# Kernel tuning notes

Hardware: AMD Instinct MI355X
Metric: run time of the kernel (lower is better)

## Reference

```python
import jax, jax.numpy as jnp
import numpy as np

EPS = 1e-5

def _bn2d(x, g, b, m, v):
    s = (1, -1, 1, 1)
    return (x - m.reshape(s)) * (g.reshape(s) * jax.lax.rsqrt(v.reshape(s) + EPS)) + b.reshape(s)

def _bn1d(x, g, b, m, v):
    return (x - m) * (g * jax.lax.rsqrt(v + EPS)) + b

def _conv3x3(x, w, b):
    y = jax.lax.conv_general_dilated(x, w, (1, 1), ((1, 1), (1, 1)),
                                     dimension_numbers=('NCHW', 'OIHW', 'NCHW'))
    return y + b.reshape(1, -1, 1, 1)

def setup_inputs() -> dict:
    key = jax.random.key(0)
    ks = iter(jax.random.split(key, 64))
    B = 512
    d = {}
    d['anchor'] = jax.random.normal(next(ks), (B, 1, 16, 8), jnp.float32)
    d['positive'] = jax.random.normal(next(ks), (B, 1, 16, 8), jnp.float32)
    d['negative'] = jax.random.normal(next(ks), (B, 1, 16, 8), jnp.float32)

    def bn_params(c):
        g = jax.random.normal(next(ks), (c,), jnp.float32) * 0.1 + 1.0
        b = jax.random.normal(next(ks), (c,), jnp.float32) * 0.1
        m = jax.random.normal(next(ks), (c,), jnp.float32) * 0.1
        v = jax.random.uniform(next(ks), (c,), jnp.float32, 0.5, 1.5)
        return g, b, m, v

    d['bn0_g'], d['bn0_b'], d['bn0_m'], d['bn0_v'] = bn_params(1)
    d['conv1_w'] = jax.random.normal(next(ks), (64, 1, 3, 3), jnp.float32) * 0.1
    d['conv1_b'] = jax.random.normal(next(ks), (64,), jnp.float32) * 0.1
    d['bn1_g'], d['bn1_b'], d['bn1_m'], d['bn1_v'] = bn_params(64)
    d['conv2_w'] = jax.random.normal(next(ks), (64, 64, 3, 3), jnp.float32) * 0.04
    d['conv2_b'] = jax.random.normal(next(ks), (64,), jnp.float32) * 0.1
    d['bn2_g'], d['bn2_b'], d['bn2_m'], d['bn2_v'] = bn_params(64)
    # locally-connected: kernel_size=1 -> per-position unshared channel mix (o,c,h,w)
    d['lc1_w'] = jax.random.normal(next(ks), (64, 64, 16, 8), jnp.float32) * 0.125
    d['bn3_g'], d['bn3_b'], d['bn3_m'], d['bn3_v'] = bn_params(64)
    d['lc2_w'] = jax.random.normal(next(ks), (64, 64, 16, 8), jnp.float32) * 0.125
    d['bn4_g'], d['bn4_b'], d['bn4_m'], d['bn4_v'] = bn_params(64)
    d['fc1_w'] = jax.random.normal(next(ks), (512, 8192), jnp.float32) * 0.01
    d['fc1_b'] = jax.random.normal(next(ks), (512,), jnp.float32) * 0.1
    d['bnf1_g'], d['bnf1_b'], d['bnf1_m'], d['bnf1_v'] = bn_params(512)
    d['fc2_w'] = jax.random.normal(next(ks), (512, 512), jnp.float32) * 0.04
    d['fc2_b'] = jax.random.normal(next(ks), (512,), jnp.float32) * 0.1
    d['bnf2_g'], d['bnf2_b'], d['bnf2_m'], d['bnf2_v'] = bn_params(512)
    d['fc3_w'] = jax.random.normal(next(ks), (128, 512), jnp.float32) * 0.04
    d['fc3_b'] = jax.random.normal(next(ks), (128,), jnp.float32) * 0.1
    d['bnf3_g'], d['bnf3_b'], d['bnf3_m'], d['bnf3_v'] = bn_params(128)
    d['out_w'] = jax.random.normal(next(ks), (128, 128), jnp.float32) * 0.09
    d['out_b'] = jax.random.normal(next(ks), (128,), jnp.float32) * 0.1
    return d

def _embedding(x, p):
    x = _bn2d(x, p['bn0_g'], p['bn0_b'], p['bn0_m'], p['bn0_v'])
    x = _conv3x3(x, p['conv1_w'], p['conv1_b'])
    x = jax.nn.relu(_bn2d(x, p['bn1_g'], p['bn1_b'], p['bn1_m'], p['bn1_v']))
    x = _conv3x3(x, p['conv2_w'], p['conv2_b'])
    x = jax.nn.relu(_bn2d(x, p['bn2_g'], p['bn2_b'], p['bn2_m'], p['bn2_v']))
    # locally connected (kernel 1): per-position channel mix, no huge unfold intermediate
    x = jnp.einsum('bchw,ochw->bohw', x, p['lc1_w'])
    x = jax.nn.relu(_bn2d(x, p['bn3_g'], p['bn3_b'], p['bn3_m'], p['bn3_v']))
    x = jnp.einsum('bchw,ochw->bohw', x, p['lc2_w'])
    x = jax.nn.relu(_bn2d(x, p['bn4_g'], p['bn4_b'], p['bn4_m'], p['bn4_v']))
    # dropout is identity in eval mode
    x = x.reshape(x.shape[0], -1)  # (B, 8192)
    x = x @ p['fc1_w'].T + p['fc1_b']
    x = jax.nn.relu(_bn1d(x, p['bnf1_g'], p['bnf1_b'], p['bnf1_m'], p['bnf1_v']))
    x = x @ p['fc2_w'].T + p['fc2_b']
    x = jax.nn.relu(_bn1d(x, p['bnf2_g'], p['bnf2_b'], p['bnf2_m'], p['bnf2_v']))
    x = x @ p['fc3_w'].T + p['fc3_b']
    x = jax.nn.relu(_bn1d(x, p['bnf3_g'], p['bnf3_b'], p['bnf3_m'], p['bnf3_v']))
    return x @ p['out_w'].T + p['out_b']

def reference(anchor, positive, negative,
              bn0_g, bn0_b, bn0_m, bn0_v,
              conv1_w, conv1_b, bn1_g, bn1_b, bn1_m, bn1_v,
              conv2_w, conv2_b, bn2_g, bn2_b, bn2_m, bn2_v,
              lc1_w, bn3_g, bn3_b, bn3_m, bn3_v,
              lc2_w, bn4_g, bn4_b, bn4_m, bn4_v,
              fc1_w, fc1_b, bnf1_g, bnf1_b, bnf1_m, bnf1_v,
              fc2_w, fc2_b, bnf2_g, bnf2_b, bnf2_m, bnf2_v,
              fc3_w, fc3_b, bnf3_g, bnf3_b, bnf3_m, bnf3_v,
              out_w, out_b):
    p = dict(bn0_g=bn0_g, bn0_b=bn0_b, bn0_m=bn0_m, bn0_v=bn0_v,
             conv1_w=conv1_w, conv1_b=conv1_b, bn1_g=bn1_g, bn1_b=bn1_b, bn1_m=bn1_m, bn1_v=bn1_v,
             conv2_w=conv2_w, conv2_b=conv2_b, bn2_g=bn2_g, bn2_b=bn2_b, bn2_m=bn2_m, bn2_v=bn2_v,
             lc1_w=lc1_w, bn3_g=bn3_g, bn3_b=bn3_b, bn3_m=bn3_m, bn3_v=bn3_v,
             lc2_w=lc2_w, bn4_g=bn4_g, bn4_b=bn4_b, bn4_m=bn4_m, bn4_v=bn4_v,
             fc1_w=fc1_w, fc1_b=fc1_b, bnf1_g=bnf1_g, bnf1_b=bnf1_b, bnf1_m=bnf1_m, bnf1_v=bnf1_v,
             fc2_w=fc2_w, fc2_b=fc2_b, bnf2_g=bnf2_g, bnf2_b=bnf2_b, bnf2_m=bnf2_m, bnf2_v=bnf2_v,
             fc3_w=fc3_w, fc3_b=fc3_b, bnf3_g=bnf3_g, bnf3_b=bnf3_b, bnf3_m=bnf3_m, bnf3_v=bnf3_v,
             out_w=out_w, out_b=out_b)
    return (_embedding(anchor, p), _embedding(positive, p), _embedding(negative, p))
```

## Files before the change

### kernel.cpp

```cpp
#include <hip/hip_runtime.h>
#include <math.h>

#define EPS 1e-5f
#define FD 8192

typedef __attribute__((ext_vector_type(8))) __bf16 bf16x8;
typedef __attribute__((ext_vector_type(4))) float f32x4;

static __device__ __forceinline__ f32x4 mfma16(bf16x8 a, bf16x8 b, f32x4 c) {
    return __builtin_amdgcn_mfma_f32_16x16x32_bf16(a, b, c, 0, 0, 0);
}

__global__ void k_prep_w1frag(const float* __restrict__ w1, __bf16* __restrict__ out) {
    const int t = threadIdx.x;
    const int lane = t & 63, w = t >> 6;
    const int q = lane >> 4, li = lane & 15;
    const int o = w * 16 + li;
    bf16x8 v;
#pragma unroll
    for (int j = 0; j < 8; ++j) {
        int k = q * 8 + j;
        v[j] = (k < 9) ? (__bf16)w1[o * 9 + k] : (__bf16)0.0f;
    }
    *(bf16x8*)(out + t * 8) = v;
}

__global__ void k_prep_w2frag(const float* __restrict__ w2, __bf16* __restrict__ out) {
    const int id = blockIdx.x * 256 + threadIdx.x;
    const int lane = id & 63;
    const int w = (id >> 6) & 3;
    const int chunk = (id >> 8) & 1;
    const int tap = id >> 9;
    const int q = lane >> 4, li = lane & 15;
    const int o = w * 16 + li;
    const int c0 = chunk * 32 + q * 8;
    bf16x8 v;
#pragma unroll
    for (int j = 0; j < 8; ++j)
        v[j] = (__bf16)w2[(o * 64 + c0 + j) * 9 + tap];
    *(bf16x8*)(out + (size_t)id * 8) = v;
}

__global__ __launch_bounds__(256) void k_prep_lcT(const float* __restrict__ lc1,
                                                  const float* __restrict__ lc2,
                                                  __bf16* __restrict__ o1,
                                                  __bf16* __restrict__ o2) {
    const int bx = blockIdx.x;
    const int layer = bx >> 6, o = bx & 63;
    const int wo = o >> 4, lo = o & 15;
    const int t = threadIdx.x;
    const float* src = (layer ? lc2 : lc1) + (size_t)o * 8192;
    __bf16* dst = layer ? o2 : o1;
    __shared__ float wbuf[64][130];
#pragma unroll
    for (int pass = 0; pass < 8; ++pass) {
        int i = pass * 1024 + t * 4;
        float4 v = *(const float4*)(src + i);
        int c = i >> 7, p = i & 127;
        wbuf[c][p + 0] = v.x; wbuf[c][p + 1] = v.y;
        wbuf[c][p + 2] = v.z; wbuf[c][p + 3] = v.w;
    }
    __syncthreads();
#pragma unroll
    for (int pass = 0; pass < 4; ++pass) {
        int slot = pass * 256 + t;
        int p = slot >> 3, chunk = (slot >> 2) & 1, q = slot & 3;
        bf16x8 v;
#pragma unroll
        for (int j = 0; j < 8; ++j)
            v[j] = (__bf16)wbuf[chunk * 32 + q * 8 + j][p];
        *(bf16x8*)(dst + ((size_t)((p * 2 + chunk) * 4 + wo) * 64 + q * 16 + lo) * 8) = v;
    }
}

__global__ __launch_bounds__(256) void k_prep_fc1T(const float* __restrict__ fw,
                                                   __bf16* __restrict__ out) {
    const int n = blockIdx.x;
    const int t = threadIdx.x;
    const float* src = fw + (size_t)n * 8192;
    __bf16* dst = out + (size_t)n * 8192;
    __shared__ float wbuf[64][130];
#pragma unroll
    for (int pass = 0; pass < 8; ++pass) {
        int i = pass * 1024 + t * 4;
        float4 v = *(const float4*)(src + i);
        int c = i >> 7, p = i & 127;
        wbuf[c][p + 0] = v.x; wbuf[c][p + 1] = v.y;
        wbuf[c][p + 2] = v.z; wbuf[c][p + 3] = v.w;
    }
    __syncthreads();
#pragma unroll
    for (int pass = 0; pass < 16; ++pass) {
        int kA = (pass * 256 + t) * 2;
        int c = kA & 63, p = kA >> 6;
        __bf16 tmp[2];
        tmp[0] = (__bf16)wbuf[c][p];
        tmp[1] = (__bf16)wbuf[c + 1][p];
        *(unsigned int*)(dst + kA) = *(unsigned int*)tmp;
    }
}

__global__ void k_cvt3(const float* __restrict__ w2, const float* __restrict__ w3,
                       const float* __restrict__ wo, __bf16* __restrict__ dst) {
    int i = blockIdx.x * 256 + threadIdx.x;
    if (i >= 344064) return;
    float v;
    if (i < 262144) v = w2[i];
    else if (i < 327680) v = w3[i - 262144];
    else v = wo[i - 327680];
    dst[i] = (__bf16)v;
}

__global__ __launch_bounds__(256) void k_conv_mfma(
    const float* __restrict__ inA, const float* __restrict__ inP, const float* __restrict__ inN,
    const float* __restrict__ bn0g, const float* __restrict__ bn0b,
    const float* __restrict__ bn0m, const float* __restrict__ bn0v,
    const __bf16* __restrict__ w1frag, const float* __restrict__ b1,
    const float* __restrict__ bn1g, const float* __restrict__ bn1b,
    const float* __restrict__ bn1m, const float* __restrict__ bn1v,
    const __bf16* __restrict__ w2frag, const float* __restrict__ b2,
    const float* __restrict__ bn2g, const float* __restrict__ bn2b,
    const float* __restrict__ bn2m, const float* __restrict__ bn2v,
    __bf16* __restrict__ act) {
    const int b = blockIdx.x, t = threadIdx.x;
    const int lane = t & 63, w = t >> 6;
    const int q = lane >> 4, li = lane & 15;
    const int n0 = w * 16;
    const float* src = (b < 512 ? inA : (b < 1024 ? inP : inN)) + (size_t)(b & 511) * 128;

    __shared__ __align__(16) float xpad[180];
    __shared__ __align__(16) __bf16 A1[128 * 40];
    __shared__ __align__(16) __bf16 Xp[18 * 12 * 72];
    __shared__ float s1[64], sh1[64], s2[64], sh2[64];

    bf16x8 w1f = *(const bf16x8*)(w1frag + (size_t)(w * 64 + lane) * 8);
    bf16x8 w2f[18];
#pragma unroll
    for (int tap = 0; tap < 9; ++tap)
#pragma unroll
        for (int ch = 0; ch < 2; ++ch)
            w2f[tap * 2 + ch] = *(const bf16x8*)(w2frag +
                ((size_t)((tap * 2 + ch) * 4 + w) * 64 + lane) * 8);

    {
        int* xz = (int*)Xp;
        for (int i = t; i < 7776; i += 256) xz[i] = 0;
        if (t < 180) xpad[t] = 0.f;
        if (t < 64) {
            float sa = bn1g[t] * rsqrtf(bn1v[t] + EPS);
            s1[t] = sa;
            sh1[t] = (b1[t] - bn1m[t]) * sa + bn1b[t];
            float sb = bn2g[t] * rsqrtf(bn2v[t] + EPS);
            s2[t] = sb;
            sh2[t] = (b2[t] - bn2m[t]) * sb + bn2b[t];
        }
    }
    __syncthreads();
    if (t < 128) {
        float s0 = bn0g[0] * rsqrtf(bn0v[0] + EPS);
        float v = (src[t] - bn0m[0]) * s0 + bn0b[0];
        xpad[((t >> 3) + 1) * 10 + (t & 7) + 1] = v;
    }
    __syncthreads();
    {
        int p = t >> 1, jh = (t & 1) * 16;
        int r = p >> 3, cl = p & 7;
#pragma unroll
        for (int jj = 0; jj < 16; ++jj) {
            int j = jh + jj;
            float v = 0.f;
            if (j < 9) v = xpad[(r + j / 3) * 10 + cl + (j % 3)];
            A1[p * 40 + j] = (__bf16)v;
        }
    }
    __syncthreads();
    {
        const float sco = s1[n0 + li], sho = sh1[n0 + li];
        const int o = n0 + li;
#pragma unroll
        for (int m = 0; m < 8; ++m) {
            bf16x8 a = *(const bf16x8*)&A1[(m * 16 + li) * 40 + q * 8];
            f32x4 z = {0.f, 0.f, 0.f, 0.f};
            f32x4 d = mfma16(a, w1f, z);
#pragma unroll
            for (int r = 0; r < 4; ++r) {
                int p = m * 16 + q * 4 + r;
                float v = fmaxf(d[r] * sco + sho, 0.f);
                Xp[(((p >> 3) + 1) * 12 + (p & 7) + 1) * 72 + o] = (__bf16)v;
            }
        }
    }
    __syncthreads();
    {
        const float sco = s2[n0 + li], sho = sh2[n0 + li];
        const int o = n0 + li;
        const int cl = li & 7;
#pragma unroll
        for (int mp = 0; mp < 4; ++mp) {
            const int m0t = mp * 2;
            const int r0 = m0t * 2 + (li >> 3);
            const int base0 = (r0 * 12 + cl) * 72 + q * 8;
            const int base1 = base0 + 1728;
            f32x4 acc0 = {0.f, 0.f, 0.f, 0.f};
            f32x4 acc1 = {0.f, 0.f, 0.f, 0.f};
#pragma unroll
            for (int tap = 0; tap < 9; ++tap) {
                const int tofs = ((tap / 3) * 12 + (tap % 3)) * 72;
#pragma unroll
                for (int ch = 0; ch < 2; ++ch) {
                    bf16x8 a0 = *(const bf16x8*)&Xp[base0 + tofs + ch * 32];
                    bf16x8 a1 = *(const bf16x8*)&Xp[base1 + tofs + ch * 32];
                    acc0 = mfma16(a0, w2f[tap * 2 + ch], acc0);
                    acc1 = mfma16(a1, w2f[tap * 2 + ch], acc1);
                }
            }
            __bf16* ob = act + (size_t)b * FD + o;
#pragma unroll
            for (int r = 0; r < 4; ++r) {
                int p0 = m0t * 16 + q * 4 + r;
                ob[p0 * 64] = (__bf16)fmaxf(acc0[r] * sco + sho, 0.f);
                ob[(p0 + 16) * 64] = (__bf16)fmaxf(acc1[r] * sco + sho, 0.f);
            }
        }
    }
}

__global__ __launch_bounds__(256) void k_lc_mfma(
    const __bf16* __restrict__ lc1frag, const __bf16* __restrict__ lc2frag,
    const float* __restrict__ bn3g, const float* __restrict__ bn3b,
    const float* __restrict__ bn3m, const float* __restrict__ bn3v,
    const float* __restrict__ bn4g, const float* __restrict__ bn4b,
    const float* __restrict__ bn4m, const float* __restrict__ bn4v,
    __bf16* __restrict__ act) {
    const int p = blockIdx.x;
    const int b0 = blockIdx.y * 64;
    const int t = threadIdx.x;
    const int lane = t & 63, w = t >> 6;
    const int q = lane >> 4, li = lane & 15;
    const int n0 = w * 16;

    __shared__ __align__(16) __bf16 xs[64 * 72];
    __shared__ __align__(16) __bf16 ys[64 * 72];
    __shared__ float s3[64], sh3[64], s4[64], sh4[64];

    if (t < 64) {
        float sa = bn3g[t] * rsqrtf(bn3v[t] + EPS);
        s3[t] = sa; sh3[t] = bn3b[t] - bn3m[t] * sa;
        float sb = bn4g[t] * rsqrtf(bn4v[t] + EPS);
        s4[t] = sb; sh4[t] = bn4b[t] - bn4m[t] * sb;
    }
    {
        int s = t >> 2, cg = t & 3;
        const __bf16* rp = act + (size_t)(b0 + s) * FD + p * 64 + cg * 16;
        *(bf16x8*)&xs[s * 72 + cg * 16] = *(const bf16x8*)rp;
        *(bf16x8*)&xs[s * 72 + cg * 16 + 8] = *(const bf16x8*)(rp + 8);
    }
    bf16x8 w1a = *(const bf16x8*)(lc1frag + ((size_t)((p * 2 + 0) * 4 + w) * 64 + lane) * 8);
    bf16x8 w1b = *(const bf16x8*)(lc1frag + ((size_t)((p * 2 + 1) * 4 + w) * 64 + lane) * 8);
    bf16x8 w2a = *(const bf16x8*)(lc2frag + ((size_t)((p * 2 + 0) * 4 + w) * 64 + lane) * 8);
    bf16x8 w2b = *(const bf16x8*)(lc2frag + ((size_t)((p * 2 + 1) * 4 + w) * 64 + lane) * 8);
    __syncthreads();
    {
        const float sco = s3[n0 + li], sho = sh3[n0 + li];
#pragma unroll
        for (int m = 0; m < 4; ++m) {
            bf16x8 a0 = *(const bf16x8*)&xs[(m * 16 + li) * 72 + q * 8];
            bf16x8 a1 = *(const bf16x8*)&xs[(m * 16 + li) * 72 + 32 + q * 8];
            f32x4 acc = {0.f, 0.f, 0.f, 0.f};
            acc = mfma16(a0, w1a, acc);
            acc = mfma16(a1, w1b, acc);
#pragma unroll
            for (int r = 0; r < 4; ++r) {
                int bl = m * 16 + q * 4 + r;
                ys[bl * 72 + n0 + li] = (__bf16)fmaxf(acc[r] * sco + sho, 0.f);
            }
        }
    }
    __syncthreads();
    {
        const float sco = s4[n0 + li], sho = sh4[n0 + li];
#pragma unroll
        for (int m = 0; m < 4; ++m) {
            bf16x8 a0 = *(const bf16x8*)&ys[(m * 16 + li) * 72 + q * 8];
            bf16x8 a1 = *(const bf16x8*)&ys[(m * 16 + li) * 72 + 32 + q * 8];
            f32x4 acc = {0.f, 0.f, 0.f, 0.f};
            acc = mfma16(a0, w2a, acc);
            acc = mfma16(a1, w2b, acc);
#pragma unroll
            for (int r = 0; r < 4; ++r) {
                int bl = m * 16 + q * 4 + r;
                act[(size_t)(b0 + bl) * FD + p * 64 + n0 + li] =
                    (__bf16)fmaxf(acc[r] * sco + sho, 0.f);
            }
        }
    }
}

__global__ __launch_bounds__(256) void k_fc1_mfma(
    const __bf16* __restrict__ A, const __bf16* __restrict__ Wb,
    float* __restrict__ part) {
    const int t = threadIdx.x;
    const int lane = t & 63, w = t >> 6;
    const int q = lane >> 4, li = lane & 15;
    const int m0 = blockIdx.x * 64, n0 = blockIdx.y * 128;
    const int k0 = blockIdx.z * 1024;
    const int wm = (w & 1) * 32, wn = (w >> 1) * 64;

    __shared__ __align__(16) __bf16 As[64 * 40];
    __shared__ __align__(16) __bf16 Bs[128 * 40];

    f32x4 acc[2][4];
#pragma unroll
    for (int i = 0; i < 2; ++i)
#pragma unroll
        for (int j = 0; j < 4; ++j) acc[i][j] = (f32x4){0.f, 0.f, 0.f, 0.f};

    const int rowA = (t & 127) >> 1, rowB = t >> 1, half = t & 1;
    const __bf16* Ag = A + (size_t)(m0 + rowA) * 8192 + k0 + half * 16;
    const __bf16* Bg = Wb + (size_t)(n0 + rowB) * 8192 + k0 + half * 16;

    for (int step = 0; step < 32; ++step) {
        bf16x8 b0 = *(const bf16x8*)Bg;
        bf16x8 b1 = *(const bf16x8*)(Bg + 8);
        if (t < 128) {
            bf16x8 a0 = *(const bf16x8*)Ag;
            bf16x8 a1 = *(const bf16x8*)(Ag + 8);
            *(bf16x8*)&As[rowA * 40 + half * 16] = a0;
            *(bf16x8*)&As[rowA * 40 + half * 16 + 8] = a1;
        }
        *(bf16x8*)&Bs[rowB * 40 + half * 16] = b0;
        *(bf16x8*)&Bs[rowB * 40 + half * 16 + 8] = b1;
        __syncthreads();
        bf16x8 af[2], bfr[4];
#pragma unroll
        for (int i = 0; i < 2; ++i)
            af[i] = *(const bf16x8*)&As[(wm + i * 16 + li) * 40 + q * 8];
#pragma unroll
        for (int j = 0; j < 4; ++j)
            bfr[j] = *(const bf16x8*)&Bs[(wn + j * 16 + li) * 40 + q * 8];
#pragma unroll
        for (int i = 0; i < 2; ++i)
#pragma unroll
            for (int j = 0; j < 4; ++j)
                acc[i][j] = mfma16(af[i], bfr[j], acc[i][j]);
        __syncthreads();
        Ag += 32;
        Bg += 32;
    }
    float* pp = part + (size_t)blockIdx.z * 786432;
#pragma unroll
    for (int i = 0; i < 2; ++i) {
#pragma unroll
        for (int r = 0; r < 4; ++r) {
            int m = m0 + wm + i * 16 + q * 4 + r;
#pragma unroll
            for (int j = 0; j < 4; ++j) {
                int n = n0 + wn + j * 16 + li;
                pp[(size_t)m * 512 + n] = acc[i][j][r];
            }
        }
    }
}

__global__ void k_fc1_reduce(const float* __restrict__ part, const float* __restrict__ bias,
                             const float* __restrict__ g, const float* __restrict__ bb,
                             const float* __restrict__ mm, const float* __restrict__ vv,
                             __bf16* __restrict__ out) {
    int gi = blockIdx.x * 256 + threadIdx.x;
    size_t off = (size_t)gi * 4;
    float4 s = make_float4(0.f, 0.f, 0.f, 0.f);
#pragma unroll
    for (int z = 0; z < 8; ++z) {
        float4 v = *(const float4*)(part + (size_t)z * 786432 + off);
        s.x += v.x; s.y += v.y; s.z += v.z; s.w += v.w;
    }
    int n = (gi & 127) * 4;
    float r[4] = {s.x, s.y, s.z, s.w};
    __bf16 o4[4];
#pragma unroll
    for (int j = 0; j < 4; ++j) {
        float sc = g[n + j] * rsqrtf(vv[n + j] + EPS);
        float x = (r[j] + bias[n + j] - mm[n + j]) * sc + bb[n + j];
        o4[j] = (__bf16)fmaxf(x, 0.f);
    }
    *(uint2*)(out + off) = *(uint2*)o4;
}

template <int FINAL>
__global__ __launch_bounds__(256) void k_fc_mfma(
    const __bf16* __restrict__ A, const __bf16* __restrict__ W,
    const float* __restrict__ bias,
    const float* __restrict__ bng, const float* __restrict__ bnb,
    const float* __restrict__ bnm, const float* __restrict__ bnv,
    void* __restrict__ out, int N, int K, int relu) {
    const int t = threadIdx.x;
    const int lane = t & 63, w = t >> 6;
    const int q = lane >> 4, li = lane & 15;
    const int m0 = blockIdx.x * 64, n0 = blockIdx.y * 64;
    const int wm = (w & 1) * 32, wn = (w >> 1) * 32;

    __shared__ __align__(16) __bf16 As[64 * 40];
    __shared__ __align__(16) __bf16 Bs[64 * 40];

    f32x4 acc[2][2];
#pragma unroll
    for (int i = 0; i < 2; ++i)
#pragma unroll
        for (int j = 0; j < 2; ++j) acc[i][j] = (f32x4){0.f, 0.f, 0.f, 0.f};

    const int row = (t & 127) >> 1, half = t & 1;
    const __bf16* g = (t < 128 ? A + (size_t)(m0 + row) * K
                               : W + (size_t)(n0 + row) * K) + half * 16;
    __bf16* ld = (t < 128 ? As : Bs) + row * 40 + half * 16;

    for (int k0 = 0; k0 < K; k0 += 32) {
        bf16x8 v0 = *(const bf16x8*)g;
        bf16x8 v1 = *(const bf16x8*)(g + 8);
        *(bf16x8*)ld = v0;
        *(bf16x8*)(ld + 8) = v1;
        __syncthreads();
        bf16x8 af[2], bfr[2];
#pragma unroll
        for (int i = 0; i < 2; ++i)
            af[i] = *(const bf16x8*)&As[(wm + i * 16 + li) * 40 + q * 8];
#pragma unroll
        for (int j = 0; j < 2; ++j)
            bfr[j] = *(const bf16x8*)&Bs[(wn + j * 16 + li) * 40 + q * 8];
#pragma unroll
        for (int i = 0; i < 2; ++i)
#pragma unroll
            for (int j = 0; j < 2; ++j)
                acc[i][j] = mfma16(af[i], bfr[j], acc[i][j]);
        __syncthreads();
        g += 32;
    }
    float bi[2], sc[2], hh[2];
#pragma unroll
    for (int j = 0; j < 2; ++j) {
        int n = n0 + wn + j * 16 + li;
        bi[j] = bias[n];
        if (bng) {
            sc[j] = bng[n] * rsqrtf(bnv[n] + EPS);
            hh[j] = bnb[n] - bnm[n] * sc[j];
        }
    }
#pragma unroll
    for (int i = 0; i < 2; ++i) {
#pragma unroll
        for (int r = 0; r < 4; ++r) {
            int m = m0 + wm + i * 16 + q * 4 + r;
#pragma unroll
            for (int j = 0; j < 2; ++j) {
                int n = n0 + wn + j * 16 + li;
                float x = acc[i][j][r] + bi[j];
                if (bng) x = x * sc[j] + hh[j];
                if (relu) x = fmaxf(x, 0.f);
                if (FINAL) ((float*)out)[(size_t)m * N + n] = x;
                else ((__bf16*)out)[(size_t)m * N + n] = (__bf16)x;
            }
        }
    }
}

extern "C" void kernel_launch(void* const* d_in, const int* in_sizes, int n_in,
                              void* d_out, int out_size, void* d_ws, size_t ws_size,
                              hipStream_t stream) {
    const float* inA    = (const float*)d_in[0];
    const float* inP    = (const float*)d_in[1];
    const float* inN    = (const float*)d_in[2];
    const float* bn0g   = (const float*)d_in[3];
    const float* bn0b   = (const float*)d_in[4];
    const float* bn0m   = (const float*)d_in[5];
    const float* bn0v   = (const float*)d_in[6];
    const float* conv1w = (const float*)d_in[7];
    const float* conv1b = (const float*)d_in[8];
    const float* bn1g   = (const float*)d_in[9];
    const float* bn1b   = (const float*)d_in[10];
    const float* bn1m   = (const float*)d_in[11];
    const float* bn1v   = (const float*)d_in[12];
    const float* conv2w = (const float*)d_in[13];
    const float* conv2b = (const float*)d_in[14];
    const float* bn2g   = (const float*)d_in[15];
    const float* bn2b   = (const float*)d_in[16];
    const float* bn2m   = (const float*)d_in[17];
    const float* bn2v   = (const float*)d_in[18];
    const float* lc1w   = (const float*)d_in[19];
    const float* bn3g   = (const float*)d_in[20];
    const float* bn3b   = (const float*)d_in[21];
    const float* bn3m   = (const float*)d_in[22];
    const float* bn3v   = (const float*)d_in[23];
    const float* lc2w   = (const float*)d_in[24];
    const float* bn4g   = (const float*)d_in[25];
    const float* bn4b   = (const float*)d_in[26];
    const float* bn4m   = (const float*)d_in[27];
    const float* bn4v   = (const float*)d_in[28];
    const float* fc1w   = (const float*)d_in[29];
    const float* fc1b   = (const float*)d_in[30];
    const float* bnf1g  = (const float*)d_in[31];
    const float* bnf1b  = (const float*)d_in[32];
    const float* bnf1m  = (const float*)d_in[33];
    const float* bnf1v  = (const float*)d_in[34];
    const float* fc2w   = (const float*)d_in[35];
    const float* fc2b   = (const float*)d_in[36];
    const float* bnf2g  = (const float*)d_in[37];
    const float* bnf2b  = (const float*)d_in[38];
    const float* bnf2m  = (const float*)d_in[39];
    const float* bnf2v  = (const float*)d_in[40];
    const float* fc3w   = (const float*)d_in[41];
    const float* fc3b   = (const float*)d_in[42];
    const float* bnf3g  = (const float*)d_in[43];
    const float* bnf3b  = (const float*)d_in[44];
    const float* bnf3m  = (const float*)d_in[45];
    const float* bnf3v  = (const float*)d_in[46];
    const float* outw   = (const float*)d_in[47];
    const float* outb   = (const float*)d_in[48];

    char* wsb = (char*)d_ws;
    __bf16* w1frag  = (__bf16*)wsb;
    __bf16* w2frag  = w1frag + 2048;
    __bf16* lc1frag = w2frag + 36864;
    __bf16* lc2frag = lc1frag + 524288;
    __bf16* fc1Wb   = lc2frag + 524288;
    __bf16* wf23    = fc1Wb + 4194304;
    __bf16* act     = wf23 + 344064;
    __bf16* act3    = act + 12582912;
    __bf16* act4    = act3 + 786432;
    __bf16* act5    = act4 + 786432;
    float*  part    = (float*)(((uintptr_t)(act5 + 196608) + 15) & ~(uintptr_t)15);
    __bf16* wf2 = wf23;
    __bf16* wf3 = wf23 + 262144;
    __bf16* wfo = wf23 + 327680;

    k_prep_w1frag<<<1, 256, 0, stream>>>(conv1w, w1frag);
    k_prep_w2frag<<<18, 256, 0, stream>>>(conv2w, w2frag);
    k_prep_lcT<<<128, 256, 0, stream>>>(lc1w, lc2w, lc1frag, lc2frag);
    k_prep_fc1T<<<512, 256, 0, stream>>>(fc1w, fc1Wb);
    k_cvt3<<<1344, 256, 0, stream>>>(fc2w, fc3w, outw, wf23);

    k_conv_mfma<<<1536, 256, 0, stream>>>(inA, inP, inN,
        bn0g, bn0b, bn0m, bn0v, w1frag, conv1b, bn1g, bn1b, bn1m, bn1v,
        w2frag, conv2b, bn2g, bn2b, bn2m, bn2v, act);

    k_lc_mfma<<<dim3(128, 24), 256, 0, stream>>>(lc1frag, lc2frag,
        bn3g, bn3b, bn3m, bn3v, bn4g, bn4b, bn4m, bn4v, act);

    k_fc1_mfma<<<dim3(24, 4, 8), 256, 0, stream>>>(act, fc1Wb, part);
    k_fc1_reduce<<<768, 256, 0, stream>>>(part, fc1b, bnf1g, bnf1b, bnf1m, bnf1v, act3);

    k_fc_mfma<0><<<dim3(24, 8), 256, 0, stream>>>(act3, wf2, fc2b,
        bnf2g, bnf2b, bnf2m, bnf2v, act4, 512, 512, 1);
    k_fc_mfma<0><<<dim3(24, 2), 256, 0, stream>>>(act4, wf3, fc3b,
        bnf3g, bnf3b, bnf3m, bnf3v, act5, 128, 512, 1);
    k_fc_mfma<1><<<dim3(24, 2), 256, 0, stream>>>(act5, wfo, outb,
        nullptr, nullptr, nullptr, nullptr, d_out, 128, 128, 0);
}
```

Measured before the change: 262.2 us.

## Merge weight-prep kernels, fuse fc3+output, stage conv/LC stores, prefetch GEMM tiles

Combines the five weight-preparation kernels into one launch that dispatches on block index. The conv and locally-connected kernels now stage their outputs in shared memory and write them back as contiguous 16-byte vectors instead of scattered 2-byte stores. The fc1 and fc2 GEMMs load the next K-tile into registers while the current one is computed. The fc3 and output layers are fused into a single kernel that keeps the intermediate activations in LDS. The aim is fewer launches and better memory coalescing, at the cost of more shared-memory use and register pressure.

```diff
diff --git a/kernel.cpp b/kernel.cpp
--- a/kernel.cpp
+++ b/kernel.cpp
@@ -11,104 +11,98 @@
     return __builtin_amdgcn_mfma_f32_16x16x32_bf16(a, b, c, 0, 0, 0);
 }
 
-__global__ void k_prep_w1frag(const float* __restrict__ w1, __bf16* __restrict__ out) {
+__global__ __launch_bounds__(256) void k_prep_all(
+    const float* __restrict__ w1, const float* __restrict__ w2,
+    const float* __restrict__ lc1, const float* __restrict__ lc2,
+    const float* __restrict__ fc1w, const float* __restrict__ fc2w,
+    const float* __restrict__ fc3w, const float* __restrict__ outw,
+    __bf16* __restrict__ w1frag, __bf16* __restrict__ w2frag,
+    __bf16* __restrict__ lc1frag, __bf16* __restrict__ lc2frag,
+    __bf16* __restrict__ fc1Wb, __bf16* __restrict__ wf23) {
+    const int bb = blockIdx.x;
     const int t = threadIdx.x;
-    const int lane = t & 63, w = t >> 6;
-    const int q = lane >> 4, li = lane & 15;
-    const int o = w * 16 + li;
-    bf16x8 v;
-#pragma unroll
-    for (int j = 0; j < 8; ++j) {
-        int k = q * 8 + j;
-        v[j] = (k < 9) ? (__bf16)w1[o * 9 + k] : (__bf16)0.0f;
-    }
-    *(bf16x8*)(out + t * 8) = v;
-}
-
-__global__ void k_prep_w2frag(const float* __restrict__ w2, __bf16* __restrict__ out) {
-    const int id = blockIdx.x * 256 + threadIdx.x;
-    const int lane = id & 63;
-    const int w = (id >> 6) & 3;
-    const int chunk = (id >> 8) & 1;
-    const int tap = id >> 9;
-    const int q = lane >> 4, li = lane & 15;
-    const int o = w * 16 + li;
-    const int c0 = chunk * 32 + q * 8;
-    bf16x8 v;
-#pragma unroll
-    for (int j = 0; j < 8; ++j)
-        v[j] = (__bf16)w2[(o * 64 + c0 + j) * 9 + tap];
-    *(bf16x8*)(out + (size_t)id * 8) = v;
-}
-
-__global__ __launch_bounds__(256) void k_prep_lcT(const float* __restrict__ lc1,
-                                                  const float* __restrict__ lc2,
-                                                  __bf16* __restrict__ o1,
-                                                  __bf16* __restrict__ o2) {
-    const int bx = blockIdx.x;
-    const int layer = bx >> 6, o = bx & 63;
-    const int wo = o >> 4, lo = o & 15;
-    const int t = threadIdx.x;
-    const float* src = (layer ? lc2 : lc1) + (size_t)o * 8192;
-    __bf16* dst = layer ? o2 : o1;
     __shared__ float wbuf[64][130];
-#pragma unroll
-    for (int pass = 0; pass < 8; ++pass) {
-        int i = pass * 1024 + t * 4;
-        float4 v = *(const float4*)(src + i);
-        int c = i >> 7, p = i & 127;
-        wbuf[c][p + 0] = v.x; wbuf[c][p + 1] = v.y;
-        wbuf[c][p + 2] = v.z; wbuf[c][p + 3] = v.w;
-    }
-    __syncthreads();
-#pragma unroll
-    for (int pass = 0; pass < 4; ++pass) {
-        int slot = pass * 256 + t;
-        int p = slot >> 3, chunk = (slot >> 2) & 1, q = slot & 3;
+
+    if (bb == 0) {
+        const int lane = t & 63, w = t >> 6;
+        const int q = lane >> 4, li = lane & 15;
+        const int o = w * 16 + li;
         bf16x8 v;
 #pragma unroll
+        for (int j = 0; j < 8; ++j) {
+            int k = q * 8 + j;
+            v[j] = (k < 9) ? (__bf16)w1[o * 9 + k] : (__bf16)0.0f;
+        }
+        *(bf16x8*)(w1frag + t * 8) = v;
+    } else if (bb < 19) {
+        const int id = (bb - 1) * 256 + t;
+        const int lane = id & 63;
+        const int w = (id >> 6) & 3;
+        const int chunk = (id >> 8) & 1;
+        const int tap = id >> 9;
+        const int q = lane >> 4, li = lane & 15;
+        const int o = w * 16 + li;
+        const int c0 = chunk * 32 + q * 8;
+        bf16x8 v;
+#pragma unroll
         for (int j = 0; j < 8; ++j)
-            v[j] = (__bf16)wbuf[chunk * 32 + q * 8 + j][p];
-        *(bf16x8*)(dst + ((size_t)((p * 2 + chunk) * 4 + wo) * 64 + q * 16 + lo) * 8) = v;
-    }
-}
-
-__global__ __launch_bounds__(256) void k_prep_fc1T(const float* __restrict__ fw,
-                                                   __bf16* __restrict__ out) {
-    const int n = blockIdx.x;
-    const int t = threadIdx.x;
-    const float* src = fw + (size_t)n * 8192;
-    __bf16* dst = out + (size_t)n * 8192;
-    __shared__ float wbuf[64][130];
-#pragma unroll
-    for (int pass = 0; pass < 8; ++pass) {
-        int i = pass * 1024 + t * 4;
-        float4 v = *(const float4*)(src + i);
-        int c = i >> 7, p = i & 127;
-        wbuf[c][p + 0] = v.x; wbuf[c][p + 1] = v.y;
-        wbuf[c][p + 2] = v.z; wbuf[c][p + 3] = v.w;
-    }
-    __syncthreads();
-#pragma unroll
-    for (int pass = 0; pass < 16; ++pass) {
-        int kA = (pass * 256 + t) * 2;
-        int c = kA & 63, p = kA >> 6;
-        __bf16 tmp[2];
-        tmp[0] = (__bf16)wbuf[c][p];
-        tmp[1] = (__bf16)wbuf[c + 1][p];
-        *(unsigned int*)(dst + kA) = *(unsigned int*)tmp;
-    }
-}
-
-__global__ void k_cvt3(const float* __restrict__ w2, const float* __restrict__ w3,
-                       const float* __restrict__ wo, __bf16* __restrict__ dst) {
-    int i = blockIdx.x * 256 + threadIdx.x;
-    if (i >= 344064) return;
-    float v;
-    if (i < 262144) v = w2[i];
-    else if (i < 327680) v = w3[i - 262144];
-    else v = wo[i - 327680];
-    dst[i] = (__bf16)v;
+            v[j] = (__bf16)w2[(o * 64 + c0 + j) * 9 + tap];
+        *(bf16x8*)(w2frag + (size_t)id * 8) = v;
+    } else if (bb < 147) {
+        const int bx = bb - 19;
+        const int layer = bx >> 6, o = bx & 63;
+        const int wo = o >> 4, lo = o & 15;
+        const float* src = (layer ? lc2 : lc1) + (size_t)o * 8192;
+        __bf16* dst = layer ? lc2frag : lc1frag;
+#pragma unroll
+        for (int pass = 0; pass < 8; ++pass) {
+            int i = pass * 1024 + t * 4;
+            float4 v = *(const float4*)(src + i);
+            int c = i >> 7, p = i & 127;
+            wbuf[c][p + 0] = v.x; wbuf[c][p + 1] = v.y;
+            wbuf[c][p + 2] = v.z; wbuf[c][p + 3] = v.w;
+        }
+        __syncthreads();
+#pragma unroll
+        for (int pass = 0; pass < 4; ++pass) {
+            int slot = pass * 256 + t;
+            int p = slot >> 3, chunk = (slot >> 2) & 1, q = slot & 3;
+            bf16x8 v;
+#pragma unroll
+            for (int j = 0; j < 8; ++j)
+                v[j] = (__bf16)wbuf[chunk * 32 + q * 8 + j][p];
+            *(bf16x8*)(dst + ((size_t)((p * 2 + chunk) * 4 + wo) * 64 + q * 16 + lo) * 8) = v;
+        }
+    } else if (bb < 659) {
+        const int n = bb - 147;
+        const float* src = fc1w + (size_t)n * 8192;
+        __bf16* dst = fc1Wb + (size_t)n * 8192;
+#pragma unroll
+        for (int pass = 0; pass < 8; ++pass) {
+            int i = pass * 1024 + t * 4;
+            float4 v = *(const float4*)(src + i);
+            int c = i >> 7, p = i & 127;
+            wbuf[c][p + 0] = v.x; wbuf[c][p + 1] = v.y;
+            wbuf[c][p + 2] = v.z; wbuf[c][p + 3] = v.w;
+        }
+        __syncthreads();
+#pragma unroll
+        for (int pass = 0; pass < 16; ++pass) {
+            int kA = (pass * 256 + t) * 2;
+            int c = kA & 63, p = kA >> 6;
+            __bf16 tmp[2];
+            tmp[0] = (__bf16)wbuf[c][p];
+            tmp[1] = (__bf16)wbuf[c + 1][p];
+            *(unsigned int*)(dst + kA) = *(unsigned int*)tmp;
+        }
+    } else {
+        int i = (bb - 659) * 256 + t;
+        float v;
+        if (i < 262144) v = fc2w[i];
+        else if (i < 327680) v = fc3w[i - 262144];
+        else v = outw[i - 327680];
+        wf23[i] = (__bf16)v;
+    }
 }
 
 __global__ __launch_bounds__(256) void k_conv_mfma(
@@ -163,15 +157,18 @@
     }
     __syncthreads();
     {
-        int p = t >> 1, jh = (t & 1) * 16;
+        int p = t >> 1, half = t & 1;
         int r = p >> 3, cl = p & 7;
-#pragma unroll
-        for (int jj = 0; jj < 16; ++jj) {
-            int j = jh + jj;
-            float v = 0.f;
-            if (j < 9) v = xpad[(r + j / 3) * 10 + cl + (j % 3)];
-            A1[p * 40 + j] = (__bf16)v;
-        }
+        bf16x8 v0, v1;
+#pragma unroll
+        for (int jj = 0; jj < 8; ++jj) {
+            int j = half * 16 + jj;
+            v0[jj] = (j < 9) ? (__bf16)xpad[(r + j / 3) * 10 + cl + (j % 3)] : (__bf16)0.f;
+            int j2 = half * 16 + 8 + jj;
+            v1[jj] = (j2 < 9) ? (__bf16)xpad[(r + j2 / 3) * 10 + cl + (j2 % 3)] : (__bf16)0.f;
+        }
+        *(bf16x8*)&A1[p * 40 + half * 16] = v0;
+        *(bf16x8*)&A1[p * 40 + half * 16 + 8] = v1;
     }
     __syncthreads();
     {
@@ -191,18 +188,19 @@
         }
     }
     __syncthreads();
-    {
-        const float sco = s2[n0 + li], sho = sh2[n0 + li];
-        const int o = n0 + li;
+    f32x4 accA[4], accB[4];
+#pragma unroll
+    for (int i = 0; i < 4; ++i) {
+        accA[i] = (f32x4){0.f, 0.f, 0.f, 0.f};
+        accB[i] = (f32x4){0.f, 0.f, 0.f, 0.f};
+    }
+    {
         const int cl = li & 7;
 #pragma unroll
         for (int mp = 0; mp < 4; ++mp) {
-            const int m0t = mp * 2;
-            const int r0 = m0t * 2 + (li >> 3);
+            const int r0 = mp * 4 + (li >> 3);
             const int base0 = (r0 * 12 + cl) * 72 + q * 8;
             const int base1 = base0 + 1728;
-            f32x4 acc0 = {0.f, 0.f, 0.f, 0.f};
-            f32x4 acc1 = {0.f, 0.f, 0.f, 0.f};
 #pragma unroll
             for (int tap = 0; tap < 9; ++tap) {
                 const int tofs = ((tap / 3) * 12 + (tap % 3)) * 72;
@@ -210,18 +208,39 @@
                 for (int ch = 0; ch < 2; ++ch) {
                     bf16x8 a0 = *(const bf16x8*)&Xp[base0 + tofs + ch * 32];
                     bf16x8 a1 = *(const bf16x8*)&Xp[base1 + tofs + ch * 32];
-                    acc0 = mfma16(a0, w2f[tap * 2 + ch], acc0);
-                    acc1 = mfma16(a1, w2f[tap * 2 + ch], acc1);
+                    accA[mp] = mfma16(a0, w2f[tap * 2 + ch], accA[mp]);
+                    accB[mp] = mfma16(a1, w2f[tap * 2 + ch], accB[mp]);
                 }
             }
-            __bf16* ob = act + (size_t)b * FD + o;
+        }
+    }
+    __syncthreads();
+    {
+        const float sco = s2[n0 + li], sho = sh2[n0 + li];
+        const int o = n0 + li;
+#pragma unroll
+        for (int mp = 0; mp < 4; ++mp) {
 #pragma unroll
             for (int r = 0; r < 4; ++r) {
-                int p0 = m0t * 16 + q * 4 + r;
-                ob[p0 * 64] = (__bf16)fmaxf(acc0[r] * sco + sho, 0.f);
-                ob[(p0 + 16) * 64] = (__bf16)fmaxf(acc1[r] * sco + sho, 0.f);
-            }
-        }
+                int p0 = mp * 32 + q * 4 + r;
+                Xp[p0 * 72 + o] = (__bf16)fmaxf(accA[mp][r] * sco + sho, 0.f);
+                Xp[(p0 + 16) * 72 + o] = (__bf16)fmaxf(accB[mp][r] * sco + sho, 0.f);
+            }
+        }
+    }
+    __syncthreads();
+    {
+        int p = t >> 1, half = t & 1;
+        const __bf16* rp = Xp + p * 72 + half * 32;
+        __bf16* ob = act + (size_t)b * FD + p * 64 + half * 32;
+        bf16x8 v0 = *(const bf16x8*)rp;
+        bf16x8 v1 = *(const bf16x8*)(rp + 8);
+        bf16x8 v2 = *(const bf16x8*)(rp + 16);
+        bf16x8 v3 = *(const bf16x8*)(rp + 24);
+        *(bf16x8*)ob = v0;
+        *(bf16x8*)(ob + 8) = v1;
+        *(bf16x8*)(ob + 16) = v2;
+        *(bf16x8*)(ob + 24) = v3;
     }
 }
 
@@ -289,10 +308,19 @@
 #pragma unroll
             for (int r = 0; r < 4; ++r) {
                 int bl = m * 16 + q * 4 + r;
-                act[(size_t)(b0 + bl) * FD + p * 64 + n0 + li] =
-                    (__bf16)fmaxf(acc[r] * sco + sho, 0.f);
-            }
-        }
+                xs[bl * 72 + n0 + li] = (__bf16)fmaxf(acc[r] * sco + sho, 0.f);
+            }
+        }
+    }
+    __syncthreads();
+    {
+        int s = t >> 2, cg = t & 3;
+        const __bf16* rp = xs + s * 72 + cg * 16;
+        __bf16* ob = act + (size_t)(b0 + s) * FD + p * 64 + cg * 16;
+        bf16x8 v0 = *(const bf16x8*)rp;
+        bf16x8 v1 = *(const bf16x8*)(rp + 8);
+        *(bf16x8*)ob = v0;
+        *(bf16x8*)(ob + 8) = v1;
     }
 }
 
@@ -319,18 +347,31 @@
     const __bf16* Ag = A + (size_t)(m0 + rowA) * 8192 + k0 + half * 16;
     const __bf16* Bg = Wb + (size_t)(n0 + rowB) * 8192 + k0 + half * 16;
 
+    bf16x8 pa0, pa1, pb0, pb1;
+    pb0 = *(const bf16x8*)Bg;
+    pb1 = *(const bf16x8*)(Bg + 8);
+    if (t < 128) {
+        pa0 = *(const bf16x8*)Ag;
+        pa1 = *(const bf16x8*)(Ag + 8);
+    }
+
     for (int step = 0; step < 32; ++step) {
-        bf16x8 b0 = *(const bf16x8*)Bg;
-        bf16x8 b1 = *(const bf16x8*)(Bg + 8);
         if (t < 128) {
-            bf16x8 a0 = *(const bf16x8*)Ag;
-            bf16x8 a1 = *(const bf16x8*)(Ag + 8);
-            *(bf16x8*)&As[rowA * 40 + half * 16] = a0;
-            *(bf16x8*)&As[rowA * 40 + half * 16 + 8] = a1;
-        }
-        *(bf16x8*)&Bs[rowB * 40 + half * 16] = b0;
-        *(bf16x8*)&Bs[rowB * 40 + half * 16 + 8] = b1;
-        __syncthreads();
+            *(bf16x8*)&As[rowA * 40 + half * 16] = pa0;
+            *(bf16x8*)&As[rowA * 40 + half * 16 + 8] = pa1;
+        }
+        *(bf16x8*)&Bs[rowB * 40 + half * 16] = pb0;
+        *(bf16x8*)&Bs[rowB * 40 + half * 16 + 8] = pb1;
+        __syncthreads();
+        Ag += 32; Bg += 32;
+        if (step < 31) {
+            pb0 = *(const bf16x8*)Bg;
+            pb1 = *(const bf16x8*)(Bg + 8);
+            if (t < 128) {
+                pa0 = *(const bf16x8*)Ag;
+                pa1 = *(const bf16x8*)(Ag + 8);
+            }
+        }
         bf16x8 af[2], bfr[4];
 #pragma unroll
         for (int i = 0; i < 2; ++i)
@@ -344,8 +385,6 @@
             for (int j = 0; j < 4; ++j)
                 acc[i][j] = mfma16(af[i], bfr[j], acc[i][j]);
         __syncthreads();
-        Ag += 32;
-        Bg += 32;
     }
     float* pp = part + (size_t)blockIdx.z * 786432;
 #pragma unroll
@@ -386,18 +425,18 @@
     *(uint2*)(out + off) = *(uint2*)o4;
 }
 
-template <int FINAL>
-__global__ __launch_bounds__(256) void k_fc_mfma(
+__global__ __launch_bounds__(256) void k_fc2_mfma(
     const __bf16* __restrict__ A, const __bf16* __restrict__ W,
     const float* __restrict__ bias,
     const float* __restrict__ bng, const float* __restrict__ bnb,
     const float* __restrict__ bnm, const float* __restrict__ bnv,
-    void* __restrict__ out, int N, int K, int relu) {
+    __bf16* __restrict__ out) {
     const int t = threadIdx.x;
     const int lane = t & 63, w = t >> 6;
     const int q = lane >> 4, li = lane & 15;
     const int m0 = blockIdx.x * 64, n0 = blockIdx.y * 64;
     const int wm = (w & 1) * 32, wn = (w >> 1) * 32;
+    const int K = 512, N = 512;
 
     __shared__ __align__(16) __bf16 As[64 * 40];
     __shared__ __align__(16) __bf16 Bs[64 * 40];
@@ -413,12 +452,17 @@
                                : W + (size_t)(n0 + row) * K) + half * 16;
     __bf16* ld = (t < 128 ? As : Bs) + row * 40 + half * 16;
 
+    bf16x8 p0 = *(const bf16x8*)g;
+    bf16x8 p1 = *(const bf16x8*)(g + 8);
     for (int k0 = 0; k0 < K; k0 += 32) {
-        bf16x8 v0 = *(const bf16x8*)g;
-        bf16x8 v1 = *(const bf16x8*)(g + 8);
-        *(bf16x8*)ld = v0;
-        *(bf16x8*)(ld + 8) = v1;
-        __syncthreads();
+        *(bf16x8*)ld = p0;
+        *(bf16x8*)(ld + 8) = p1;
+        __syncthreads();
+        g += 32;
+        if (k0 + 32 < K) {
+            p0 = *(const bf16x8*)g;
+            p1 = *(const bf16x8*)(g + 8);
+        }
         bf16x8 af[2], bfr[2];
 #pragma unroll
         for (int i = 0; i < 2; ++i)
@@ -432,17 +476,14 @@
             for (int j = 0; j < 2; ++j)
                 acc[i][j] = mfma16(af[i], bfr[j], acc[i][j]);
         __syncthreads();
-        g += 32;
     }
     float bi[2], sc[2], hh[2];
 #pragma unroll
     for (int j = 0; j < 2; ++j) {
         int n = n0 + wn + j * 16 + li;
         bi[j] = bias[n];
-        if (bng) {
-            sc[j] = bng[n] * rsqrtf(bnv[n] + EPS);
-            hh[j] = bnb[n] - bnm[n] * sc[j];
-        }
+        sc[j] = bng[n] * rsqrtf(bnv[n] + EPS);
+        hh[j] = bnb[n] - bnm[n] * sc[j];
     }
 #pragma unroll
     for (int i = 0; i < 2; ++i) {
@@ -452,13 +493,132 @@
 #pragma unroll
             for (int j = 0; j < 2; ++j) {
                 int n = n0 + wn + j * 16 + li;
-                float x = acc[i][j][r] + bi[j];
-                if (bng) x = x * sc[j] + hh[j];
-                if (relu) x = fmaxf(x, 0.f);
-                if (FINAL) ((float*)out)[(size_t)m * N + n] = x;
-                else ((__bf16*)out)[(size_t)m * N + n] = (__bf16)x;
-            }
-        }
+                float x = (acc[i][j][r] + bi[j]) * sc[j] + hh[j];
+                out[(size_t)m * N + n] = (__bf16)fmaxf(x, 0.f);
+            }
+        }
+    }
+}
+
+__global__ __launch_bounds__(256) void k_fc3out(
+    const __bf16* __restrict__ A, const __bf16* __restrict__ W3,
+    const __bf16* __restrict__ Wo,
+    const float* __restrict__ b3,
+    const float* __restrict__ bng, const float* __restrict__ bnb,
+    const float* __restrict__ bnm, const float* __restrict__ bnv,
+    const float* __restrict__ bo, float* __restrict__ out) {
+    const int t = threadIdx.x;
+    const int lane = t & 63, w = t >> 6;
+    const int q = lane >> 4, li = lane & 15;
+    const int m0 = blockIdx.x * 64;
+    const int wn = w * 32;
+
+    __shared__ __align__(16) __bf16 As[64 * 40];
+    __shared__ __align__(16) __bf16 Bs[128 * 40];
+    __shared__ __align__(16) __bf16 ysb[64 * 136];
+
+    const int rowA = (t & 127) >> 1, rowB = t >> 1, half = t & 1;
+    const __bf16* Ag = A + (size_t)(m0 + rowA) * 512 + half * 16;
+    const __bf16* Bg = W3 + (size_t)rowB * 512 + half * 16;
+
+    f32x4 acc[4][2];
+#pragma unroll
+    for (int i = 0; i < 4; ++i)
+#pragma unroll
+        for (int j = 0; j < 2; ++j) acc[i][j] = (f32x4){0.f, 0.f, 0.f, 0.f};
+
+    bf16x8 pa0, pa1, pb0, pb1;
+    pb0 = *(const bf16x8*)Bg;
+    pb1 = *(const bf16x8*)(Bg + 8);
+    if (t < 128) {
+        pa0 = *(const bf16x8*)Ag;
+        pa1 = *(const bf16x8*)(Ag + 8);
+    }
+    for (int step = 0; step < 16; ++step) {
+        if (t < 128) {
+            *(bf16x8*)&As[rowA * 40 + half * 16] = pa0;
+            *(bf16x8*)&As[rowA * 40 + half * 16 + 8] = pa1;
+        }
+        *(bf16x8*)&Bs[rowB * 40 + half * 16] = pb0;
+        *(bf16x8*)&Bs[rowB * 40 + half * 16 + 8] = pb1;
+        __syncthreads();
+        Ag += 32; Bg += 32;
+        if (step < 15) {
+            pb0 = *(const bf16x8*)Bg;
+            pb1 = *(const bf16x8*)(Bg + 8);
+            if (t < 128) {
+                pa0 = *(const bf16x8*)Ag;
+                pa1 = *(const bf16x8*)(Ag + 8);
+            }
+        }
+        bf16x8 af[4], bfr[2];
+#pragma unroll
+        for (int i = 0; i < 4; ++i)
+            af[i] = *(const bf16x8*)&As[(i * 16 + li) * 40 + q * 8];
+#pragma unroll
+        for (int j = 0; j < 2; ++j)
+            bfr[j] = *(const bf16x8*)&Bs[(wn + j * 16 + li) * 40 + q * 8];
+#pragma unroll
+        for (int i = 0; i < 4; ++i)
+#pragma unroll
+            for (int j = 0; j < 2; ++j)
+                acc[i][j] = mfma16(af[i], bfr[j], acc[i][j]);
+        __syncthreads();
+    }
+    {
+#pragma unroll
+        for (int j = 0; j < 2; ++j) {
+            int n = wn + j * 16 + li;
+            float sc = bng[n] * rsqrtf(bnv[n] + EPS);
+            float hh = bnb[n] - bnm[n] * sc;
+            float bi = b3[n];
+#pragma unroll
+            for (int i = 0; i < 4; ++i)
+#pragma unroll
+                for (int r = 0; r < 4; ++r) {
+                    int ml = i * 16 + q * 4 + r;
+                    float x = (acc[i][j][r] + bi) * sc + hh;
+                    ysb[ml * 136 + n] = (__bf16)fmaxf(x, 0.f);
+                }
+        }
+    }
+    __syncthreads();
+    f32x4 acc2[4][2];
+#pragma unroll
+    for (int i = 0; i < 4; ++i)
+#pragma unroll
+        for (int j = 0; j < 2; ++j) acc2[i][j] = (f32x4){0.f, 0.f, 0.f, 0.f};
+    const __bf16* Bg2 = Wo + (size_t)rowB * 128 + half * 16;
+#pragma unroll
+    for (int step = 0; step < 4; ++step) {
+        *(bf16x8*)&Bs[rowB * 40 + half * 16] = *(const bf16x8*)(Bg2 + step * 32);
+        *(bf16x8*)&Bs[rowB * 40 + half * 16 + 8] = *(const bf16x8*)(Bg2 + step * 32 + 8);
+        __syncthreads();
+        bf16x8 af[4], bfr[2];
+#pragma unroll
+        for (int i = 0; i < 4; ++i)
+            af[i] = *(const bf16x8*)&ysb[(i * 16 + li) * 136 + step * 32 + q * 8];
+#pragma unroll
+        for (int j = 0; j < 2; ++j)
+            bfr[j] = *(const bf16x8*)&Bs[(wn + j * 16 + li) * 40 + q * 8];
+#pragma unroll
+        for (int i = 0; i < 4; ++i)
+#pragma unroll
+            for (int j = 0; j < 2; ++j)
+                acc2[i][j] = mfma16(af[i], bfr[j], acc2[i][j]);
+        __syncthreads();
+    }
+#pragma unroll
+    for (int j = 0; j < 2; ++j) {
+        int n = wn + j * 16 + li;
+        float bi = bo[n];
+#pragma unroll
+        for (int i = 0; i < 4; ++i)
+#pragma unroll
+            for (int r = 0; r < 4; ++r) {
+                int m = m0 + i * 16 + q * 4 + r;
+                out[(size_t)m * 128 + n] = acc2[i][j][r] + bi;
+            }
     }
 }
 
@@ -525,17 +685,13 @@
     __bf16* act     = wf23 + 344064;
     __bf16* act3    = act + 12582912;
     __bf16* act4    = act3 + 786432;
-    __bf16* act5    = act4 + 786432;
-    float*  part    = (float*)(((uintptr_t)(act5 + 196608) + 15) & ~(uintptr_t)15);
+    float*  part    = (float*)(((uintptr_t)(act4 + 786432) + 15) & ~(uintptr_t)15);
     __bf16* wf2 = wf23;
     __bf16* wf3 = wf23 + 262144;
     __bf16* wfo = wf23 + 327680;
 
-    k_prep_w1frag<<<1, 256, 0, stream>>>(conv1w, w1frag);
-    k_prep_w2frag<<<18, 256, 0, stream>>>(conv2w, w2frag);
-    k_prep_lcT<<<128, 256, 0, stream>>>(lc1w, lc2w, lc1frag, lc2frag);
-    k_prep_fc1T<<<512, 256, 0, stream>>>(fc1w, fc1Wb);
-    k_cvt3<<<1344, 256, 0, stream>>>(fc2w, fc3w, outw, wf23);
+    k_prep_all<<<2003, 256, 0, stream>>>(conv1w, conv2w, lc1w, lc2w,
+        fc1w, fc2w, fc3w, outw, w1frag, w2frag, lc1frag, lc2frag, fc1Wb, wf23);
 
     k_conv_mfma<<<1536, 256, 0, stream>>>(inA, inP, inN,
         bn0g, bn0b, bn0m, bn0v, w1frag, conv1b, bn1g, bn1b, bn1m, bn1v,
@@ -547,10 +703,9 @@
     k_fc1_mfma<<<dim3(24, 4, 8), 256, 0, stream>>>(act, fc1Wb, part);
     k_fc1_reduce<<<768, 256, 0, stream>>>(part, fc1b, bnf1g, bnf1b, bnf1m, bnf1v, act3);
 
-    k_fc_mfma<0><<<dim3(24, 8), 256, 0, stream>>>(act3, wf2, fc2b,
-        bnf2g, bnf2b, bnf2m, bnf2v, act4, 512, 512, 1);
-    k_fc_mfma<0><<<dim3(24, 2), 256, 0, stream>>>(act4, wf3, fc3b,
-        bnf3g, bnf3b, bnf3m, bnf3v, act5, 128, 512, 1);
-    k_fc_mfma<1><<<dim3(24, 2), 256, 0, stream>>>(act5, wfo, outb,
-        nullptr, nullptr, nullptr, nullptr, d_out, 128, 128, 0);
-}
+    k_fc2_mfma<<<dim3(24, 8), 256, 0, stream>>>(act3, wf2, fc2b,
+        bnf2g, bnf2b, bnf2m, bnf2v, act4);
+
+    k_fc3out<<<24, 256, 0, stream>>>(act4, wf3, wfo, fc3b,
+        bnf3g, bnf3b, bnf3m, bnf3v, outb, (float*)d_out);
+}
```

Result: faster. 250.8 us (-4.4%).
